# Performance work log

Measured on AMD Instinct MI355X. Metric: run time of the kernel, lower is better.

The kernel has to match this reference:

```python
import jax, jax.numpy as jnp
import numpy as np

# ---- constants derived from init_kwargs ----
DETECT_THRESHOLD = 3.0
DETECT_SIGN = -1          # negative spikes
MARGIN_LEFT = 20          # snippet_T1
MARGIN_RIGHT = 20         # snippet_T2
CHANNEL_RADIUS = 100.0
SAMPLING_FREQUENCY = 30000.0
TIME_RADIUS = int(np.ceil(0.5 / 1000.0 * SAMPLING_FREQUENCY))  # = 15
MAX_DETECTIONS = 100000   # static cap for jit-compatible compaction


def setup_inputs() -> dict:
    key = jax.random.key(0)
    k1, k2 = jax.random.split(key)
    traces = jax.random.normal(k1, (150000, 384), dtype=jnp.float32)
    # spread channels over a 2000x2000 um area so radius=100 gives sparse adjacency
    channel_locations = jax.random.uniform(k2, (384, 2), dtype=jnp.float32) * 2000.0
    return {"traces": traces, "channel_locations": channel_locations}


def _detect_mask(traces, channel_locations):
    N, M = traces.shape
    # orientation (detect_sign < 0 -> traces_inv = -traces)
    if DETECT_SIGN > 0:
        traces_inv = traces
    elif DETECT_SIGN == 0:
        traces_inv = jnp.abs(traces)
    else:
        traces_inv = -traces

    # temporal max-pool, kernel 2*TR+1, stride 1, same padding (pads with -inf)
    pool = 2 * TIME_RADIUS + 1
    neg_inf = jnp.float32(-jnp.inf)
    temporal_max = jax.lax.reduce_window(
        traces_inv, neg_inf, jax.lax.max,
        window_dimensions=(pool, 1), window_strides=(1, 1),
        padding=((TIME_RADIUS, TIME_RADIUS), (0, 0)))  # [N, M]

    # channel adjacency from pairwise distances
    diff = channel_locations[:, None, :] - channel_locations[None, :, :]
    dists = jnp.sqrt(jnp.sum(diff * diff, axis=-1))  # [M, M]
    adj = dists <= CHANNEL_RADIUS

    # per-channel masked neighbor max over temporal_max columns -> [N, M]
    # sequential lax.map over channels avoids an N x M x M intermediate
    spatial_max = jax.lax.map(
        lambda row: jnp.max(jnp.where(row[None, :], temporal_max, neg_inf), axis=1),
        adj).T  # [N, M]

    t = jnp.arange(N)
    margin_ok = (t >= MARGIN_LEFT) & (t < N - MARGIN_RIGHT)  # [N]

    valid = ((traces_inv == temporal_max)
             & (traces_inv >= DETECT_THRESHOLD)
             & margin_ok[:, None]
             & (traces_inv >= spatial_max))
    return valid, traces_inv


def reference(traces, channel_locations):
    valid, _ = _detect_mask(traces, channel_locations)
    # row-major nonzero order == stable sort by time (row index)
    times, chans = jnp.nonzero(valid, size=MAX_DETECTIONS, fill_value=-1)
    return times.astype(jnp.int64), chans.astype(jnp.int32)
```

## Files before the change

### kernel.cpp

```cpp
#include <hip/hip_runtime.h>
#include <stdint.h>

#define M_CH      384
#define THRESH    3.0f
#define MARGIN    20
#define TR        15
#define CHUNK     16
#define HALO      46
#define BM_WORDS  192

__global__ void nbr_kernel(const float* __restrict__ locs,
                           uint32_t* __restrict__ nbrCount,
                           uint16_t* __restrict__ nbrList) {
    __shared__ float lx[M_CH], ly[M_CH];
    int t = threadIdx.x;
    lx[t] = locs[2 * t];
    ly[t] = locs[2 * t + 1];
    __syncthreads();
    float x = lx[t], y = ly[t];
    int cnt = 0;
    for (int c = 0; c < M_CH; ++c) {
        float dx = x - lx[c], dy = y - ly[c];
        float d = sqrtf(dx * dx + dy * dy);
        if (d <= 100.0f) { nbrList[t * M_CH + cnt] = (uint16_t)c; cnt++; }
    }
    nbrCount[t] = cnt;
}

__global__ __launch_bounds__(384, 3)
void detect_kernel(const float* __restrict__ traces, int N,
                   const uint32_t* __restrict__ nbrCount,
                   const uint16_t* __restrict__ nbrList,
                   uint32_t* __restrict__ bitmask,
                   uint32_t* __restrict__ chunkCounts)
{
    __shared__ float HB[HALO * M_CH];
    __shared__ uint32_t bm[BM_WORDS];
    __shared__ uint32_t cnt;

    const int t = threadIdx.x;
    const int c = t;
    const int chunk = blockIdx.x;
    const int r0 = chunk * CHUNK;

    if (t < BM_WORDS) bm[t] = 0;
    if (t == 0) cnt = 0;

    const int rloc = t / 96;
    const int col4 = t - rloc * 96;
    #pragma unroll
    for (int k = 0; k < 12; ++k) {
        int row = k * 4 + rloc;
        if (row < HALO) {
            int grow = r0 - TR + row;
            grow = min(max(grow, 0), N - 1);
            float4 v = *(const float4*)(traces + (long)grow * M_CH + col4 * 4);
            *(float4*)(&HB[row * M_CH + col4 * 4]) = v;
        }
    }
    __syncthreads();

    float w[HALO];
    #pragma unroll
    for (int j = 0; j < HALO; ++j) w[j] = HB[j * M_CH + c];

    float raw[CHUNK];
    #pragma unroll
    for (int n = 0; n < CHUNK; ++n) raw[n] = w[n + TR];

    #pragma unroll
    for (int j = 0; j < HALO - 1; ++j)  w[j] = fminf(w[j], w[j + 1]);
    #pragma unroll
    for (int j = 0; j < HALO - 3; ++j)  w[j] = fminf(w[j], w[j + 2]);
    #pragma unroll
    for (int j = 0; j < HALO - 7; ++j)  w[j] = fminf(w[j], w[j + 4]);
    #pragma unroll
    for (int j = 0; j < HALO - 15; ++j) w[j] = fminf(w[j], w[j + 8]);

    __syncthreads();

    #pragma unroll
    for (int n = 0; n < CHUNK; ++n)
        HB[n * M_CH + c] = fminf(w[n], w[n + TR]);
    __syncthreads();

    uint32_t cand = 0;
    #pragma unroll
    for (int n = 0; n < CHUNK; ++n) {
        int row = r0 + n;
        if (row >= MARGIN && row < N - MARGIN && raw[n] <= -THRESH)
            cand |= (1u << n);
    }
    const int nnb = (int)nbrCount[c];
    while (cand) {
        int n = __ffs(cand) - 1;
        cand &= cand - 1;
        float rv = raw[n];
        bool ok = true;
        for (int j = 0; j < nnb; ++j) {
            int c2 = (int)nbrList[c * M_CH + j];
            if (rv > HB[n * M_CH + c2]) { ok = false; break; }
        }
        if (ok) {
            int f = n * M_CH + c;
            atomicOr(&bm[f >> 5], 1u << (f & 31));
        }
    }
    __syncthreads();

    if (t < BM_WORDS) {
        uint32_t wv = bm[t];
        bitmask[(long)chunk * BM_WORDS + t] = wv;
        if (wv) atomicAdd(&cnt, (uint32_t)__popc(wv));
    }
    __syncthreads();
    if (t == 0) chunkCounts[chunk] = cnt;
}

__global__ void scan_kernel(const uint32_t* __restrict__ counts, int n,
                            uint32_t* __restrict__ prefix) {
    __shared__ uint32_t s[256];
    int t = threadIdx.x;
    int per = (n + 255) / 256;
    int lo = t * per, hi = min(lo + per, n);
    uint32_t sum = 0;
    for (int i = lo; i < hi; ++i) sum += counts[i];
    s[t] = sum;
    __syncthreads();
    for (int off = 1; off < 256; off <<= 1) {
        uint32_t v = (t >= off) ? s[t - off] : 0;
        __syncthreads();
        s[t] += v;
        __syncthreads();
    }
    uint32_t run = s[t] - sum;
    for (int i = lo; i < hi; ++i) { prefix[i] = run; run += counts[i]; }
    if (t == 255) prefix[n] = run;
}

__global__ void emit_kernel(const uint32_t* __restrict__ bitmask,
                            const uint32_t* __restrict__ chunkPrefix,
                            int nchunk, int maxdet,
                            int* __restrict__ times, int* __restrict__ chans) {
    int wv = threadIdx.x >> 6;
    int lane = threadIdx.x & 63;
    int chunkId = blockIdx.x * 4 + wv;
    if (chunkId >= nchunk) return;

    const uint32_t* wp = bitmask + (long)chunkId * BM_WORDS + lane * 3;
    uint32_t b0 = wp[0], b1 = wp[1], b2 = wp[2];
    int p0 = __popc(b0), p1 = __popc(b1), p2 = __popc(b2);
    int local = p0 + p1 + p2;

    int s = local;
    #pragma unroll
    for (int off = 1; off < 64; off <<= 1) {
        int v = __shfl_up(s, off, 64);
        if (lane >= off) s += v;
    }
    int base = (int)chunkPrefix[chunkId] + (s - local);
    int r0 = chunkId * CHUNK;

    uint32_t words[3] = { b0, b1, b2 };
    #pragma unroll
    for (int q = 0; q < 3; ++q) {
        uint32_t x = words[q];
        int fbase = (lane * 3 + q) * 32;
        while (x) {
            int b = __ffs(x) - 1;
            x &= x - 1;
            int f = fbase + b;
            int n = f / M_CH;
            int ch = f - n * M_CH;
            if (base < maxdet) {
                times[base] = r0 + n;
                chans[base] = ch;
            }
            base++;
        }
    }
}

__global__ void fill_kernel(const uint32_t* __restrict__ totalPtr, int maxdet,
                            int* __restrict__ times, int* __restrict__ chans) {
    int i = blockIdx.x * blockDim.x + threadIdx.x;
    int total = (int)*totalPtr;
    if (i < maxdet && i >= total) { times[i] = -1; chans[i] = -1; }
}

extern "C" void kernel_launch(void* const* d_in, const int* in_sizes, int n_in,
                              void* d_out, int out_size, void* d_ws, size_t ws_size,
                              hipStream_t stream) {
    const float* traces = (const float*)d_in[0];
    const float* locs   = (const float*)d_in[1];
    const int M = M_CH;
    const int N = in_sizes[0] / M;
    const int maxdet = out_size / 2;
    int* times = (int*)d_out;
    int* chans = times + maxdet;

    const int nchunk = (N + CHUNK - 1) / CHUNK;
    char* ws = (char*)d_ws;
    uint32_t* nbrCount    = (uint32_t*)ws;
    uint16_t* nbrList     = (uint16_t*)(ws + 1536);
    uint32_t* chunkCounts = (uint32_t*)(ws + 1536 + 294912);
    uint32_t* chunkPrefix = chunkCounts + nchunk;
    uint32_t* bitmask     = chunkPrefix + nchunk + 1;

    nbr_kernel<<<1, M_CH, 0, stream>>>(locs, nbrCount, nbrList);

    detect_kernel<<<nchunk, M_CH, 0, stream>>>(traces, N, nbrCount, nbrList,
                                               bitmask, chunkCounts);

    scan_kernel<<<1, 256, 0, stream>>>(chunkCounts, nchunk, chunkPrefix);

    emit_kernel<<<(nchunk + 3) / 4, 256, 0, stream>>>(bitmask, chunkPrefix,
                                                      nchunk, maxdet,
                                                      times, chans);

    fill_kernel<<<(maxdet + 255) / 256, 256, 0, stream>>>(chunkPrefix + nchunk,
                                                          maxdet, times, chans);
}
```

Before: 511.7 us.

## Split detection into threshold candidate pass and sparse worklist validation

Replaces the dense per-chunk detect kernel, which computed a temporal sliding min for every sample, with a streaming threshold pass. That pass writes a candidate bitmask and appends nonzero 32-bit words to a global worklist through atomics. A second kernel validates each candidate with a wavefront that reads the full spatio-temporal neighborhood directly from global memory. The aim is to avoid the full temporal pooling work and shared-memory staging, since threshold crossings are sparse. The cost is extra kernel launches, global atomics, uncoalesced gather reads for validation, and a fixed worklist cap.

```diff
diff --git a/kernel.cpp b/kernel.cpp
--- a/kernel.cpp
+++ b/kernel.cpp
@@ -1,13 +1,12 @@
 #include <hip/hip_runtime.h>
 #include <stdint.h>
 
-#define M_CH      384
-#define THRESH    3.0f
-#define MARGIN    20
-#define TR        15
-#define CHUNK     16
-#define HALO      46
-#define BM_WORDS  192
+#define M_CH       384
+#define TR         15
+#define MARGIN     20
+#define CHUNK_ROWS 16
+#define BM_WORDS   192
+#define WLCAP      262144
 
 __global__ void nbr_kernel(const float* __restrict__ locs,
                            uint32_t* __restrict__ nbrCount,
@@ -27,94 +26,90 @@
     nbrCount[t] = cnt;
 }
 
-__global__ __launch_bounds__(384, 3)
-void detect_kernel(const float* __restrict__ traces, int N,
-                   const uint32_t* __restrict__ nbrCount,
-                   const uint16_t* __restrict__ nbrList,
-                   uint32_t* __restrict__ bitmask,
-                   uint32_t* __restrict__ chunkCounts)
-{
-    __shared__ float HB[HALO * M_CH];
-    __shared__ uint32_t bm[BM_WORDS];
-    __shared__ uint32_t cnt;
-
-    const int t = threadIdx.x;
-    const int c = t;
-    const int chunk = blockIdx.x;
-    const int r0 = chunk * CHUNK;
-
-    if (t < BM_WORDS) bm[t] = 0;
-    if (t == 0) cnt = 0;
-
-    const int rloc = t / 96;
-    const int col4 = t - rloc * 96;
+__global__ void init_kernel(uint32_t* __restrict__ wlCount) {
+    if (threadIdx.x == 0) *wlCount = 0;
+}
+
+__global__ __launch_bounds__(256)
+void cand_kernel(const float* __restrict__ traces, int mlo8, int mhi8,
+                 uint8_t* __restrict__ candBytes,
+                 uint32_t* __restrict__ wlCount,
+                 uint32_t* __restrict__ worklist) {
+    int t = blockIdx.x * 256 + threadIdx.x;
+    const float4* p = (const float4*)traces + (long)t * 2;
+    float4 a = p[0], b = p[1];
+    uint32_t m = 0;
+    if (t >= mlo8 && t < mhi8) {
+        m |= (a.x <= -3.0f) ? 1u   : 0u;
+        m |= (a.y <= -3.0f) ? 2u   : 0u;
+        m |= (a.z <= -3.0f) ? 4u   : 0u;
+        m |= (a.w <= -3.0f) ? 8u   : 0u;
+        m |= (b.x <= -3.0f) ? 16u  : 0u;
+        m |= (b.y <= -3.0f) ? 32u  : 0u;
+        m |= (b.z <= -3.0f) ? 64u  : 0u;
+        m |= (b.w <= -3.0f) ? 128u : 0u;
+    }
+    candBytes[t] = (uint8_t)m;
+    uint64_t bal = __ballot(m != 0);
+    int lane = threadIdx.x & 63;
+    if ((lane & 3) == 0) {
+        if ((bal >> lane) & 0xFull) {
+            uint32_t slot = atomicAdd(wlCount, 1u);
+            if (slot < WLCAP) worklist[slot] = (uint32_t)(t >> 2);
+        }
+    }
+}
+
+__global__ __launch_bounds__(256)
+void validate_kernel(const float* __restrict__ traces,
+                     const uint32_t* __restrict__ nbrCount,
+                     const uint16_t* __restrict__ nbrList,
+                     uint32_t* __restrict__ candBits,
+                     const uint32_t* __restrict__ wlCount,
+                     const uint32_t* __restrict__ worklist) {
+    int lane = threadIdx.x & 63;
+    int wid  = (blockIdx.x * 256 + threadIdx.x) >> 6;
+    int nw   = (gridDim.x * 256) >> 6;
+    uint32_t cnt = min(*wlCount, (uint32_t)WLCAP);
+    for (uint32_t e = wid; e < cnt; e += nw) {
+        uint32_t idx = worklist[e];
+        uint32_t word = candBits[idx];
+        int r  = (int)(idx / 12);
+        int c0 = ((int)idx - r * 12) * 32;
+        uint32_t tmp = word;
+        while (tmp) {
+            int b = __ffs(tmp) - 1;
+            tmp &= tmp - 1;
+            int c = c0 + b;
+            float raw = traces[(long)r * M_CH + c];
+            int nnb = (int)nbrCount[c];
+            int total = nnb * 31;
+            float mn = INFINITY;
+            for (int i = lane; i < total; i += 64) {
+                int j  = i / 31;
+                int dt = i - j * 31 - TR;
+                int c2 = (int)nbrList[c * M_CH + j];
+                mn = fminf(mn, traces[(long)(r + dt) * M_CH + c2]);
+            }
+            #pragma unroll
+            for (int off = 32; off; off >>= 1)
+                mn = fminf(mn, __shfl_xor(mn, off, 64));
+            if (raw > mn) word &= ~(1u << b);
+        }
+        if (lane == 0) candBits[idx] = word;
+    }
+}
+
+__global__ void count_kernel(const uint32_t* __restrict__ candBits, int nchunk,
+                             uint32_t* __restrict__ chunkCounts) {
+    int lane  = threadIdx.x & 63;
+    int chunk = (blockIdx.x * blockDim.x + threadIdx.x) >> 6;
+    if (chunk >= nchunk) return;
+    const uint32_t* wp = candBits + (long)chunk * BM_WORDS;
+    int s = __popc(wp[lane]) + __popc(wp[lane + 64]) + __popc(wp[lane + 128]);
     #pragma unroll
-    for (int k = 0; k < 12; ++k) {
-        int row = k * 4 + rloc;
-        if (row < HALO) {
-            int grow = r0 - TR + row;
-            grow = min(max(grow, 0), N - 1);
-            float4 v = *(const float4*)(traces + (long)grow * M_CH + col4 * 4);
-            *(float4*)(&HB[row * M_CH + col4 * 4]) = v;
-        }
-    }
-    __syncthreads();
-
-    float w[HALO];
-    #pragma unroll
-    for (int j = 0; j < HALO; ++j) w[j] = HB[j * M_CH + c];
-
-    float raw[CHUNK];
-    #pragma unroll
-    for (int n = 0; n < CHUNK; ++n) raw[n] = w[n + TR];
-
-    #pragma unroll
-    for (int j = 0; j < HALO - 1; ++j)  w[j] = fminf(w[j], w[j + 1]);
-    #pragma unroll
-    for (int j = 0; j < HALO - 3; ++j)  w[j] = fminf(w[j], w[j + 2]);
-    #pragma unroll
-    for (int j = 0; j < HALO - 7; ++j)  w[j] = fminf(w[j], w[j + 4]);
-    #pragma unroll
-    for (int j = 0; j < HALO - 15; ++j) w[j] = fminf(w[j], w[j + 8]);
-
-    __syncthreads();
-
-    #pragma unroll
-    for (int n = 0; n < CHUNK; ++n)
-        HB[n * M_CH + c] = fminf(w[n], w[n + TR]);
-    __syncthreads();
-
-    uint32_t cand = 0;
-    #pragma unroll
-    for (int n = 0; n < CHUNK; ++n) {
-        int row = r0 + n;
-        if (row >= MARGIN && row < N - MARGIN && raw[n] <= -THRESH)
-            cand |= (1u << n);
-    }
-    const int nnb = (int)nbrCount[c];
-    while (cand) {
-        int n = __ffs(cand) - 1;
-        cand &= cand - 1;
-        float rv = raw[n];
-        bool ok = true;
-        for (int j = 0; j < nnb; ++j) {
-            int c2 = (int)nbrList[c * M_CH + j];
-            if (rv > HB[n * M_CH + c2]) { ok = false; break; }
-        }
-        if (ok) {
-            int f = n * M_CH + c;
-            atomicOr(&bm[f >> 5], 1u << (f & 31));
-        }
-    }
-    __syncthreads();
-
-    if (t < BM_WORDS) {
-        uint32_t wv = bm[t];
-        bitmask[(long)chunk * BM_WORDS + t] = wv;
-        if (wv) atomicAdd(&cnt, (uint32_t)__popc(wv));
-    }
-    __syncthreads();
-    if (t == 0) chunkCounts[chunk] = cnt;
+    for (int off = 32; off; off >>= 1) s += __shfl_xor(s, off, 64);
+    if (lane == 0) chunkCounts[chunk] = (uint32_t)s;
 }
 
 __global__ void scan_kernel(const uint32_t* __restrict__ counts, int n,
@@ -138,7 +133,7 @@
     if (t == 255) prefix[n] = run;
 }
 
-__global__ void emit_kernel(const uint32_t* __restrict__ bitmask,
+__global__ void emit_kernel(const uint32_t* __restrict__ candBits,
                             const uint32_t* __restrict__ chunkPrefix,
                             int nchunk, int maxdet,
                             int* __restrict__ times, int* __restrict__ chans) {
@@ -147,10 +142,9 @@
     int chunkId = blockIdx.x * 4 + wv;
     if (chunkId >= nchunk) return;
 
-    const uint32_t* wp = bitmask + (long)chunkId * BM_WORDS + lane * 3;
+    const uint32_t* wp = candBits + (long)chunkId * BM_WORDS + lane * 3;
     uint32_t b0 = wp[0], b1 = wp[1], b2 = wp[2];
-    int p0 = __popc(b0), p1 = __popc(b1), p2 = __popc(b2);
-    int local = p0 + p1 + p2;
+    int local = __popc(b0) + __popc(b1) + __popc(b2);
 
     int s = local;
     #pragma unroll
@@ -159,7 +153,7 @@
         if (lane >= off) s += v;
     }
     int base = (int)chunkPrefix[chunkId] + (s - local);
-    int r0 = chunkId * CHUNK;
+    int r0 = chunkId * CHUNK_ROWS;
 
     uint32_t words[3] = { b0, b1, b2 };
     #pragma unroll
@@ -195,26 +189,41 @@
     const float* locs   = (const float*)d_in[1];
     const int M = M_CH;
     const int N = in_sizes[0] / M;
+    const int nsamp = N * M;
     const int maxdet = out_size / 2;
     int* times = (int*)d_out;
     int* chans = times + maxdet;
 
-    const int nchunk = (N + CHUNK - 1) / CHUNK;
+    const int nchunk = (N + CHUNK_ROWS - 1) / CHUNK_ROWS;
+
     char* ws = (char*)d_ws;
-    uint32_t* nbrCount    = (uint32_t*)ws;
+    uint32_t* nbrCount    = (uint32_t*)(ws + 0);
     uint16_t* nbrList     = (uint16_t*)(ws + 1536);
-    uint32_t* chunkCounts = (uint32_t*)(ws + 1536 + 294912);
-    uint32_t* chunkPrefix = chunkCounts + nchunk;
-    uint32_t* bitmask     = chunkPrefix + nchunk + 1;
-
+    uint32_t* wlCount     = (uint32_t*)(ws + 296448);
+    uint32_t* chunkCounts = (uint32_t*)(ws + 296464);
+    uint32_t* chunkPrefix = (uint32_t*)(ws + 333968);
+    uint32_t* worklist    = (uint32_t*)(ws + 371472);
+    uint32_t* candBits    = (uint32_t*)(ws + 1420048);
+    uint8_t*  candBytes   = (uint8_t*)candBits;
+
+    init_kernel<<<1, 64, 0, stream>>>(wlCount);
     nbr_kernel<<<1, M_CH, 0, stream>>>(locs, nbrCount, nbrList);
 
-    detect_kernel<<<nchunk, M_CH, 0, stream>>>(traces, N, nbrCount, nbrList,
-                                               bitmask, chunkCounts);
+    const int ngroups = nsamp / 8;
+    const int mlo8 = (MARGIN * M) / 8;
+    const int mhi8 = ((N - MARGIN) * M) / 8;
+    cand_kernel<<<ngroups / 256, 256, 0, stream>>>(traces, mlo8, mhi8,
+                                                   candBytes, wlCount, worklist);
+
+    validate_kernel<<<2048, 256, 0, stream>>>(traces, nbrCount, nbrList,
+                                              candBits, wlCount, worklist);
+
+    count_kernel<<<(nchunk * 64 + 255) / 256, 256, 0, stream>>>(candBits, nchunk,
+                                                                chunkCounts);
 
     scan_kernel<<<1, 256, 0, stream>>>(chunkCounts, nchunk, chunkPrefix);
 
-    emit_kernel<<<(nchunk + 3) / 4, 256, 0, stream>>>(bitmask, chunkPrefix,
+    emit_kernel<<<(nchunk + 3) / 4, 256, 0, stream>>>(candBits, chunkPrefix,
                                                       nchunk, maxdet,
                                                       times, chans);
 
```

Result: slower. 1.089 ms (+112.8%).
